# Performance work log

Hardware: AMD Instinct MI355X
Metric: run time of the kernel (lower is better)

## Reference

```python
import jax, jax.numpy as jnp
import numpy as np

N = 50000   # nodes
E = 800000  # edges (avg_degree 16)
C = 64      # channels
R = 8       # radial basis
H = 64      # radial MLP hidden
S = 10      # species
AVG_NUM_NEIGHBORS = 16.0


def setup_inputs() -> dict:
    key = jax.random.key(0)
    ks = jax.random.split(key, 16)
    node_feats0 = jax.random.normal(ks[0], (N, C), jnp.float32)
    node_feats1 = jax.random.normal(ks[1], (N, C, 3), jnp.float32)
    species = jax.random.randint(ks[2], (N,), 0, S)
    node_attrs = jax.nn.one_hot(species, S, dtype=jnp.float32)
    edge_index = jax.random.randint(ks[3], (2, E), 0, N)
    edge_feats = jax.random.normal(ks[4], (E, R), jnp.float32)
    vec = jax.random.normal(ks[5], (E, 3), jnp.float32)
    edge_attrs1 = vec / (jnp.linalg.norm(vec, axis=-1, keepdims=True) + 1e-9)
    cutoff = jax.random.uniform(ks[6], (E, 1), jnp.float32)
    Wup0 = jax.random.normal(ks[7], (C, C), jnp.float32) * (C ** -0.5)
    Wup1 = jax.random.normal(ks[8], (C, C), jnp.float32) * (C ** -0.5)
    W1 = jax.random.normal(ks[9], (R, H), jnp.float32) * (R ** -0.5)
    W2 = jax.random.normal(ks[10], (H, 4 * C), jnp.float32) * (H ** -0.5)
    Wsc0 = jax.random.normal(ks[11], (S, C, C), jnp.float32) * (C ** -0.5)
    Wsc1 = jax.random.normal(ks[12], (S, C, C), jnp.float32) * (C ** -0.5)
    Q0 = jnp.eye(1, dtype=jnp.float32)   # ICTD(0,0) projector
    Q1 = jnp.eye(3, dtype=jnp.float32)   # ICTD(1,1) projector
    return dict(node_feats0=node_feats0, node_feats1=node_feats1,
                node_attrs=node_attrs, edge_feats=edge_feats,
                edge_attrs1=edge_attrs1, cutoff=cutoff,
                Wup0=Wup0, Wup1=Wup1, W1=W1, W2=W2,
                Wsc0=Wsc0, Wsc1=Wsc1, Q0=Q0, Q1=Q1,
                edge_index=edge_index)


def reference(node_feats0, node_feats1, node_attrs, edge_feats, edge_attrs1,
              cutoff, Wup0, Wup1, W1, W2, Wsc0, Wsc1, Q0, Q1, edge_index):
    n = node_feats0.shape[0]
    src, dst = edge_index[0], edge_index[1]
    # linear_up (SelfInteraction): per-degree channel mixing
    h0 = node_feats0 @ Wup0                                   # [N,C]
    h1 = jnp.einsum('nci,co->noi', node_feats1, Wup1)         # [N,C,3]
    # radial MLP -> per-path per-channel edge weights
    w = jax.nn.silu(edge_feats @ W1) @ W2                     # [E,4C]
    w00, w11, w01, w10 = jnp.split(w, 4, axis=-1)             # each [E,C]
    # gather sender features per edge
    h0e = h0[src]                                             # [E,C]
    h1e = h1[src]                                             # [E,C,3]
    sh1 = edge_attrs1                                         # [E,3]
    # equivariant tensor-product paths, cutoff-modulated (Contraction)
    m0 = (w00 * h0e + w11 * jnp.einsum('eci,ei->ec', h1e, sh1)) * cutoff
    m1 = (w01[:, :, None] * h0e[:, :, None] * sh1[:, None, :]
          + w10[:, :, None] * h1e) * cutoff[:, :, None]       # [E,C,3]
    # scatter to receiver nodes + fixed normalizer
    T0 = jax.ops.segment_sum(m0, dst, num_segments=n) / AVG_NUM_NEIGHBORS
    T1 = jax.ops.segment_sum(m1, dst, num_segments=n) / AVG_NUM_NEIGHBORS
    # ICTD decomposition projection: T.reshape(B,C,-1) @ Q
    mi0 = (T0[:, :, None] @ Q0)[:, :, 0]                      # [N,C]
    mi1 = T1 @ Q1                                             # [N,C,3]
    # residual via ElementLinear (per-species channel mixing)
    res0 = jnp.einsum('ns,sco,nc->no', node_attrs, Wsc0, mi0)
    res1 = jnp.einsum('ns,sco,nci->noi', node_attrs, Wsc1, mi1)
    return jnp.concatenate(
        [mi0, mi1.reshape(n, 3 * C), res0, res1.reshape(n, 3 * C)], axis=-1)
```

## Files before the change

kernel.cpp:

```cpp
#include <hip/hip_runtime.h>
#include <math.h>


#define NB 16
#define TE 32

__device__ __forceinline__ float silu(float x) {
    return x / (1.0f + __expf(-x));
}

__global__ __launch_bounds__(256) void up_kernel(
    const float* __restrict__ nf0, const float* __restrict__ nf1,
    const float* __restrict__ Wup0, const float* __restrict__ Wup1,
    float* __restrict__ out, int Nn) {
    __shared__ float sW0[4096];
    __shared__ float sW1u[4096];
    __shared__ float s0[4 * 64];
    __shared__ float s1[4 * 192];
    int t = threadIdx.x;
    for (int i = t; i < 4096; i += 256) { sW0[i] = Wup0[i]; sW1u[i] = Wup1[i]; }
    int n0 = blockIdx.x * 4;
    {
        int n = n0 + (t >> 6);
        s0[t] = (n < Nn) ? nf0[(size_t)n * 64 + (t & 63)] : 0.f;
    }
    for (int i = t; i < 768; i += 256) {
        int n = n0 + i / 192;
        s1[i] = (n < Nn) ? nf1[(size_t)n * 192 + (i % 192)] : 0.f;
    }
    __syncthreads();
    int w = t >> 6, o = t & 63;
    int n = n0 + w;
    if (n >= Nn) return;
    float a0 = 0.f, ax = 0.f, ay = 0.f, az = 0.f;
#pragma unroll 8
    for (int c = 0; c < 64; c++) {
        float w0 = sW0[c * 64 + o];
        float w1 = sW1u[c * 64 + o];
        float f0 = s0[w * 64 + c];
        a0 += f0 * w0;
        ax += s1[w * 192 + c * 3 + 0] * w1;
        ay += s1[w * 192 + c * 3 + 1] * w1;
        az += s1[w * 192 + c * 3 + 2] * w1;
    }
    float* row = out + (size_t)n * 512;
    row[256 + o] = a0;
    row[320 + o * 3 + 0] = ax;
    row[320 + o * 3 + 1] = ay;
    row[320 + o * 3 + 2] = az;
}

__global__ __launch_bounds__(256) void hist_kernel(
    const int* __restrict__ ei, int* __restrict__ cnt, int E) {
    int e = blockIdx.x * 256 + threadIdx.x;
    if (e < E) atomicAdd(&cnt[ei[(size_t)E + e]], 1);
}

__global__ __launch_bounds__(1024) void scan_kernel(
    int* __restrict__ cnt, int* __restrict__ cur, int Nn, int E) {
    __shared__ int wsum[16];
    __shared__ int carry_s;
    int t = threadIdx.x;
    int lane = t & 63, wid = t >> 6;
    if (t == 0) carry_s = 0;
    __syncthreads();
    int nchunk = (Nn + 1023) >> 10;
    for (int ch = 0; ch < nchunk; ch++) {
        int i = (ch << 10) + t;
        int v = (i < Nn) ? cnt[i] : 0;
        int s = v;
#pragma unroll
        for (int d = 1; d < 64; d <<= 1) {
            int u = __shfl_up(s, d);
            if (lane >= d) s += u;
        }
        if (lane == 63) wsum[wid] = s;
        __syncthreads();
        int carry = carry_s;
        if (wid == 0) {
            int x = (lane < 16) ? wsum[lane] : 0;
#pragma unroll
            for (int d = 1; d < 16; d <<= 1) {
                int u = __shfl_up(x, d);
                if (lane >= d) x += u;
            }
            if (lane < 16) wsum[lane] = x;
        }
        __syncthreads();
        int woff = wid ? wsum[wid - 1] : 0;
        int excl = carry + woff + (s - v);
        if (i < Nn) { cnt[i] = excl; cur[i] = excl; }
        __syncthreads();
        if (t == 1023) carry_s = carry + wsum[15];
        __syncthreads();
    }
    if (t == 0) cnt[Nn] = E;
}

__global__ __launch_bounds__(256) void fill_kernel(
    const int* __restrict__ ei, int* __restrict__ cur, int* __restrict__ csr, int E) {
    int e = blockIdx.x * 256 + threadIdx.x;
    if (e < E) {
        int pos = atomicAdd(&cur[ei[(size_t)E + e]], 1);
        csr[pos] = e;
    }
}

#define FMA4(A, S, B) { (A).x += (S)*(B).x; (A).y += (S)*(B).y; (A).z += (S)*(B).z; (A).w += (S)*(B).w; }

__global__ __launch_bounds__(256, 1) void gather_kernel(
    const float* __restrict__ edge_feats, const float* __restrict__ edge_attrs1,
    const float* __restrict__ cutoff, const int* __restrict__ ei,
    const int* __restrict__ offs, const int* __restrict__ csr,
    const float* __restrict__ W1g, const float* __restrict__ W2g,
    float* __restrict__ out, int Nn, int E) {
    __shared__ __align__(16) float sW1[512];
    __shared__ __align__(16) float sW2[64 * 256];
    __shared__ __align__(16) float h_t[TE * 68];
    __shared__ __align__(16) float h0_t[TE * 68];
    __shared__ __align__(16) float h1_t[TE * 196];
    __shared__ __align__(16) float w_t[TE * 260];
    __shared__ __align__(16) float accs[NB * 256];
    __shared__ __align__(16) float4 meta4[TE];
    __shared__ int dstl[TE];
    int t = threadIdx.x;

    for (int i = t; i < 512; i += 256) sW1[i] = W1g[i];
    {
        float4* d4 = reinterpret_cast<float4*>(sW2);
        const float4* s4 = reinterpret_cast<const float4*>(W2g);
        for (int i = t; i < 4096; i += 256) d4[i] = s4[i];
    }
    for (int i = t; i < NB * 256; i += 256) accs[i] = 0.f;
    int n0 = blockIdx.x * NB;
    int nend = n0 + NB; if (nend > Nn) nend = Nn;
    int pbeg = offs[n0];
    int pend = offs[nend];
    __syncthreads();

    int e0 = t >> 3, q = t & 7;
    int g = t >> 5, cs = t & 31;
    int wv = t >> 6, c = t & 63;
    int off2 = (wv == 0) ? c : (64 + c * 3 + (wv - 1));

    const float4* h4  = reinterpret_cast<const float4*>(h_t);
    const float4* w24 = reinterpret_cast<const float4*>(sW2);
    float4* wt4 = reinterpret_cast<float4*>(w_t);

    float racc = 0.f;
    int prev = -1;

    for (int tb = pbeg; tb < pend; tb += TE) {
        int n_t = pend - tb; if (n_t > TE) n_t = TE;

        if (e0 < n_t) {
            int eg = csr[tb + e0];
            int src = ei[eg];
            if (q == 0) {
                dstl[e0] = ei[(size_t)E + eg] - n0;
                meta4[e0] = make_float4(edge_attrs1[(size_t)eg * 3 + 0],
                                        edge_attrs1[(size_t)eg * 3 + 1],
                                        edge_attrs1[(size_t)eg * 3 + 2],
                                        cutoff[eg]);
            }
            const float4* h0g = reinterpret_cast<const float4*>(out + (size_t)src * 512 + 256);
            const float4* h1g = reinterpret_cast<const float4*>(out + (size_t)src * 512 + 320);
            float4 ga = h0g[2 * q], gb = h0g[2 * q + 1];
            *reinterpret_cast<float4*>(&h0_t[e0 * 68 + q * 8]) = ga;
            *reinterpret_cast<float4*>(&h0_t[e0 * 68 + q * 8 + 4]) = gb;
#pragma unroll
            for (int k = 0; k < 6; k++) {
                float4 v = h1g[6 * q + k];
                *reinterpret_cast<float4*>(&h1_t[e0 * 196 + q * 24 + k * 4]) = v;
            }
            const float4* efp = reinterpret_cast<const float4*>(edge_feats + (size_t)eg * 8);
            float4 efa = efp[0], efb = efp[1];
            float hv0 = 0.f, hv1 = 0.f, hv2 = 0.f, hv3 = 0.f;
            float hv4 = 0.f, hv5 = 0.f, hv6 = 0.f, hv7 = 0.f;
            float4 wva, wvb;
#define H8(EFR, RR) \
            wva = *reinterpret_cast<const float4*>(&sW1[(RR) * 64 + q * 8]); \
            wvb = *reinterpret_cast<const float4*>(&sW1[(RR) * 64 + q * 8 + 4]); \
            hv0 += (EFR) * wva.x; hv1 += (EFR) * wva.y; hv2 += (EFR) * wva.z; hv3 += (EFR) * wva.w; \
            hv4 += (EFR) * wvb.x; hv5 += (EFR) * wvb.y; hv6 += (EFR) * wvb.z; hv7 += (EFR) * wvb.w;
            H8(efa.x, 0) H8(efa.y, 1) H8(efa.z, 2) H8(efa.w, 3)
            H8(efb.x, 4) H8(efb.y, 5) H8(efb.z, 6) H8(efb.w, 7)
#undef H8
            float4 o1 = make_float4(silu(hv0), silu(hv1), silu(hv2), silu(hv3));
            float4 o2 = make_float4(silu(hv4), silu(hv5), silu(hv6), silu(hv7));
            *reinterpret_cast<float4*>(&h_t[e0 * 68 + q * 8]) = o1;
            *reinterpret_cast<float4*>(&h_t[e0 * 68 + q * 8 + 4]) = o2;
        }
        __syncthreads();

        {
            float4 accA0 = {0,0,0,0}, accA1 = {0,0,0,0}, accA2 = {0,0,0,0}, accA3 = {0,0,0,0};
            float4 accB0 = {0,0,0,0}, accB1 = {0,0,0,0}, accB2 = {0,0,0,0}, accB3 = {0,0,0,0};
            int eb = g * 4;
#pragma unroll 4
            for (int lq = 0; lq < 16; lq++) {
                float4 ha0 = h4[(eb + 0) * 17 + lq];
                float4 ha1 = h4[(eb + 1) * 17 + lq];
                float4 ha2 = h4[(eb + 2) * 17 + lq];
                float4 ha3 = h4[(eb + 3) * 17 + lq];
#define S1LI(LI, CMP) { \
                float4 wA = w24[(lq * 4 + LI) * 64 + cs]; \
                float4 wB = w24[(lq * 4 + LI) * 64 + 32 + cs]; \
                FMA4(accA0, ha0.CMP, wA) FMA4(accB0, ha0.CMP, wB) \
                FMA4(accA1, ha1.CMP, wA) FMA4(accB1, ha1.CMP, wB) \
                FMA4(accA2, ha2.CMP, wA) FMA4(accB2, ha2.CMP, wB) \
                FMA4(accA3, ha3.CMP, wA) FMA4(accB3, ha3.CMP, wB) }
                S1LI(0, x) S1LI(1, y) S1LI(2, z) S1LI(3, w)
#undef S1LI
            }
            wt4[(eb + 0) * 65 + cs] = accA0; wt4[(eb + 0) * 65 + 32 + cs] = accB0;
            wt4[(eb + 1) * 65 + cs] = accA1; wt4[(eb + 1) * 65 + 32 + cs] = accB1;
            wt4[(eb + 2) * 65 + cs] = accA2; wt4[(eb + 2) * 65 + 32 + cs] = accB2;
            wt4[(eb + 3) * 65 + cs] = accA3; wt4[(eb + 3) * 65 + 32 + cs] = accB3;
        }
        __syncthreads();

        for (int e = 0; e < n_t; e++) {
            int d = dstl[e];
            float4 m = meta4[e];
            if (d != prev) {
                if (prev >= 0) atomicAdd(&accs[prev * 256 + off2], racc);
                racc = 0.f;
                prev = d;
            }
            float h0e = h0_t[e * 68 + c];
            if (wv == 0) {
                float w00 = w_t[e * 260 + c];
                float w11 = w_t[e * 260 + 64 + c];
                float x1 = h1_t[e * 196 + c * 3 + 0];
                float y1 = h1_t[e * 196 + c * 3 + 1];
                float z1 = h1_t[e * 196 + c * 3 + 2];
                float dd = x1 * m.x + y1 * m.y + z1 * m.z;
                racc += (w00 * h0e + w11 * dd) * m.w;
            } else {
                int i = wv - 1;
                float w01 = w_t[e * 260 + 128 + c];
                float w10 = w_t[e * 260 + 192 + c];
                float h1i = h1_t[e * 196 + c * 3 + i];
                float shi = (wv == 1) ? m.x : ((wv == 2) ? m.y : m.z);
                racc += (w01 * h0e * shi + w10 * h1i) * m.w;
            }
        }
        __syncthreads();
    }
    if (prev >= 0) atomicAdd(&accs[prev * 256 + off2], racc);
    __syncthreads();

    for (int i = t; i < NB * 256; i += 256) {
        int ln = i >> 8, idx = i & 255;
        if (n0 + ln < Nn) out[(size_t)(n0 + ln) * 512 + idx] = accs[i];
    }
}

__global__ __launch_bounds__(256, 2) void edge_kernel(
    const float* __restrict__ edge_feats, const float* __restrict__ edge_attrs1,
    const float* __restrict__ cutoff, const int* __restrict__ edge_index,
    const float* __restrict__ W1g, const float* __restrict__ W2g,
    float* __restrict__ out, int E) {
    __shared__ __align__(16) float sW1[8 * 64];
    __shared__ __align__(16) float sW2[64 * 256];
    int t = threadIdx.x;
    sW1[t] = W1g[t];
    sW1[t + 256] = W1g[t + 256];
    for (int i = t; i < 16384; i += 256) sW2[i] = W2g[i];
    __syncthreads();

    int e = blockIdx.x * 256 + t;
    if (e >= E) return;

    float ef[8];
    {
        const float4* p = reinterpret_cast<const float4*>(edge_feats + (size_t)e * 8);
        float4 a = p[0], b = p[1];
        ef[0] = a.x; ef[1] = a.y; ef[2] = a.z; ef[3] = a.w;
        ef[4] = b.x; ef[5] = b.y; ef[6] = b.z; ef[7] = b.w;
    }
    float h[64];
#pragma unroll
    for (int hg = 0; hg < 16; hg++) {
        float ax = 0.f, ay = 0.f, az = 0.f, aw = 0.f;
#pragma unroll
        for (int rr = 0; rr < 8; rr++) {
            const float4 wv = *reinterpret_cast<const float4*>(&sW1[rr * 64 + hg * 4]);
            ax += ef[rr] * wv.x; ay += ef[rr] * wv.y;
            az += ef[rr] * wv.z; aw += ef[rr] * wv.w;
        }
        h[hg * 4 + 0] = silu(ax);
        h[hg * 4 + 1] = silu(ay);
        h[hg * 4 + 2] = silu(az);
        h[hg * 4 + 3] = silu(aw);
    }

    int src = edge_index[e];
    int dst = edge_index[(size_t)E + e];
    float cut = cutoff[e];
    float sh0 = edge_attrs1[(size_t)e * 3 + 0];
    float sh1v = edge_attrs1[(size_t)e * 3 + 1];
    float sh2 = edge_attrs1[(size_t)e * 3 + 2];
    const float* h0r = out + (size_t)src * 512 + 256;
    const float* h1r = out + (size_t)src * 512 + 320;
    float* outr = out + (size_t)dst * 512;
    const float4* w2v = reinterpret_cast<const float4*>(sW2);

#pragma unroll 1
    for (int cg = 0; cg < 16; cg++) {
        float a00[4] = {0.f, 0.f, 0.f, 0.f};
        float a11[4] = {0.f, 0.f, 0.f, 0.f};
        float a01[4] = {0.f, 0.f, 0.f, 0.f};
        float a10[4] = {0.f, 0.f, 0.f, 0.f};
#pragma unroll
        for (int l = 0; l < 64; l++) {
            float hl = h[l];
            float4 w00v = w2v[l * 64 + cg];
            float4 w11v = w2v[l * 64 + 16 + cg];
            float4 w01v = w2v[l * 64 + 32 + cg];
            float4 w10v = w2v[l * 64 + 48 + cg];
            a00[0] += hl * w00v.x; a00[1] += hl * w00v.y; a00[2] += hl * w00v.z; a00[3] += hl * w00v.w;
            a11[0] += hl * w11v.x; a11[1] += hl * w11v.y; a11[2] += hl * w11v.z; a11[3] += hl * w11v.w;
            a01[0] += hl * w01v.x; a01[1] += hl * w01v.y; a01[2] += hl * w01v.z; a01[3] += hl * w01v.w;
            a10[0] += hl * w10v.x; a10[1] += hl * w10v.y; a10[2] += hl * w10v.z; a10[3] += hl * w10v.w;
        }
        int c0 = cg * 4;
        float4 h0v = *reinterpret_cast<const float4*>(h0r + c0);
        float4 q0 = *reinterpret_cast<const float4*>(h1r + c0 * 3);
        float4 q1 = *reinterpret_cast<const float4*>(h1r + c0 * 3 + 4);
        float4 q2 = *reinterpret_cast<const float4*>(h1r + c0 * 3 + 8);
        float h0a[4] = {h0v.x, h0v.y, h0v.z, h0v.w};
        float h1a[12] = {q0.x, q0.y, q0.z, q0.w, q1.x, q1.y, q1.z, q1.w,
                         q2.x, q2.y, q2.z, q2.w};
#pragma unroll
        for (int k = 0; k < 4; k++) {
            int c = c0 + k;
            float he0 = h0a[k];
            float e0 = h1a[k * 3 + 0], e1 = h1a[k * 3 + 1], e2 = h1a[k * 3 + 2];
            float d = e0 * sh0 + e1 * sh1v + e2 * sh2;
            float m0 = (a00[k] * he0 + a11[k] * d) * cut;
            atomicAdd(outr + c, m0);
            float wa = a01[k] * he0 * cut;
            float wb = a10[k] * cut;
            atomicAdd(outr + 64 + c * 3 + 0, wa * sh0 + wb * e0);
            atomicAdd(outr + 64 + c * 3 + 1, wa * sh1v + wb * e1);
            atomicAdd(outr + 64 + c * 3 + 2, wa * sh2 + wb * e2);
        }
    }
}

__global__ __launch_bounds__(256) void finalize_kernel(
    const float* __restrict__ node_attrs, const float* __restrict__ Wsc0,
    const float* __restrict__ Wsc1, const float* __restrict__ Q0,
    const float* __restrict__ Q1, float* __restrict__ out, int Nn) {
    __shared__ float smi0[4][64];
    __shared__ float smi1[4][192];
    int t = threadIdx.x;
    int w = t >> 6, o = t & 63;
    int n = blockIdx.x * 4 + w;
    const float inv = 1.0f / 16.0f;
    float q00 = Q0[0];
    float Q[9];
#pragma unroll
    for (int i = 0; i < 9; i++) Q[i] = Q1[i];
    if (n < Nn) {
        float* row = out + (size_t)n * 512;
        float t0 = row[o];
        float ta = row[64 + o * 3 + 0];
        float tb = row[64 + o * 3 + 1];
        float tc = row[64 + o * 3 + 2];
        float mi0 = t0 * inv * q00;
        float m0i = inv * (ta * Q[0] + tb * Q[3] + tc * Q[6]);
        float m1i = inv * (ta * Q[1] + tb * Q[4] + tc * Q[7]);
        float m2i = inv * (ta * Q[2] + tb * Q[5] + tc * Q[8]);
        row[o] = mi0;
        row[64 + o * 3 + 0] = m0i;
        row[64 + o * 3 + 1] = m1i;
        row[64 + o * 3 + 2] = m2i;
        smi0[w][o] = mi0;
        smi1[w][o * 3 + 0] = m0i;
        smi1[w][o * 3 + 1] = m1i;
        smi1[w][o * 3 + 2] = m2i;
    }
    __syncthreads();
    if (n >= Nn) return;
    float acc0 = 0.f, acc1x = 0.f, acc1y = 0.f, acc1z = 0.f;
    for (int s = 0; s < 10; s++) {
        float a = node_attrs[(size_t)n * 10 + s];
        if (a != 0.f) {
            const float* w0 = Wsc0 + s * 4096;
            const float* w1 = Wsc1 + s * 4096;
            float p0 = 0.f, px = 0.f, py = 0.f, pz = 0.f;
#pragma unroll 8
            for (int c = 0; c < 64; c++) {
                float v0 = w0[c * 64 + o];
                float v1 = w1[c * 64 + o];
                p0 += smi0[w][c] * v0;
                px += smi1[w][c * 3 + 0] * v1;
                py += smi1[w][c * 3 + 1] * v1;
                pz += smi1[w][c * 3 + 2] * v1;
            }
            acc0 += a * p0; acc1x += a * px; acc1y += a * py; acc1z += a * pz;
        }
    }
    float* row = out + (size_t)n * 512;
    row[256 + o] = acc0;
    row[320 + o * 3 + 0] = acc1x;
    row[320 + o * 3 + 1] = acc1y;
    row[320 + o * 3 + 2] = acc1z;
}

extern "C" void kernel_launch(void* const* d_in, const int* in_sizes, int n_in,
                              void* d_out, int out_size, void* d_ws, size_t ws_size,
                              hipStream_t stream) {
    const float* nf0   = (const float*)d_in[0];
    const float* nf1   = (const float*)d_in[1];
    const float* attrs = (const float*)d_in[2];
    const float* ef    = (const float*)d_in[3];
    const float* ea1   = (const float*)d_in[4];
    const float* cut   = (const float*)d_in[5];
    const float* Wup0  = (const float*)d_in[6];
    const float* Wup1  = (const float*)d_in[7];
    const float* W1    = (const float*)d_in[8];
    const float* W2    = (const float*)d_in[9];
    const float* Wsc0  = (const float*)d_in[10];
    const float* Wsc1  = (const float*)d_in[11];
    const float* Q0    = (const float*)d_in[12];
    const float* Q1    = (const float*)d_in[13];
    const int*   ei    = (const int*)d_in[14];
    int Nn = in_sizes[0] / 64;
    int E  = in_sizes[14] / 2;
    float* out = (float*)d_out;

    size_t need_bytes = ((size_t)(2 * Nn + 1) + (size_t)E) * sizeof(int);
    int ebl = (E + 255) / 256;

    if (d_ws != nullptr && ws_size >= need_bytes) {
        int* cnt = (int*)d_ws;
        int* cur = cnt + (Nn + 1);
        int* csr = cur + Nn;
        hipMemsetAsync(cnt, 0, (size_t)(Nn + 1) * sizeof(int), stream);
        hist_kernel<<<ebl, 256, 0, stream>>>(ei, cnt, E);
        scan_kernel<<<1, 1024, 0, stream>>>(cnt, cur, Nn, E);
        fill_kernel<<<ebl, 256, 0, stream>>>(ei, cur, csr, E);
        up_kernel<<<(Nn + 3) / 4, 256, 0, stream>>>(nf0, nf1, Wup0, Wup1, out, Nn);
        gather_kernel<<<(Nn + NB - 1) / NB, 256, 0, stream>>>(
            ef, ea1, cut, ei, cnt, csr, W1, W2, out, Nn, E);
        finalize_kernel<<<(Nn + 3) / 4, 256, 0, stream>>>(attrs, Wsc0, Wsc1, Q0, Q1, out, Nn);
    } else {
        hipMemsetAsync(out, 0, (size_t)out_size * sizeof(float), stream);
        up_kernel<<<(Nn + 3) / 4, 256, 0, stream>>>(nf0, nf1, Wup0, Wup1, out, Nn);
        edge_kernel<<<ebl, 256, 0, stream>>>(ef, ea1, cut, ei, W1, W2, out, E);
        finalize_kernel<<<(Nn + 3) / 4, 256, 0, stream>>>(attrs, Wsc0, Wsc1, Q0, Q1, out, Nn);
    }
}
```

Baseline: 1.825 ms.

## Prefetch next edge tile into registers and split scatter loop across waves by edge

Gathers for the next edge tile (source node features, edge features, attrs, cutoff, destination) are issued into registers right after the first barrier, so their global latency overlaps the W2 matmul stage of the current tile. The scatter-accumulate loop changes from each wave owning one output component over all edges to each wave taking every fourth edge and computing all four outputs. This removes redundant shared-memory reads and loop iterations per wave, but gives more flush points, issuing four shared atomics per destination change instead of one. The prefetch also raises register pressure under the 256-thread launch bound.

Result: faster. 1.605 ms (-12.1%).

```diff
diff --git a/kernel.cpp b/kernel.cpp
--- a/kernel.cpp
+++ b/kernel.cpp
@@ -141,40 +141,58 @@
     int e0 = t >> 3, q = t & 7;
     int g = t >> 5, cs = t & 31;
     int wv = t >> 6, c = t & 63;
-    int off2 = (wv == 0) ? c : (64 + c * 3 + (wv - 1));
 
     const float4* h4  = reinterpret_cast<const float4*>(h_t);
     const float4* w24 = reinterpret_cast<const float4*>(sW2);
     float4* wt4 = reinterpret_cast<float4*>(w_t);
 
-    float racc = 0.f;
+    float r0 = 0.f, rx = 0.f, ry = 0.f, rz = 0.f;
     int prev = -1;
 
-    for (int tb = pbeg; tb < pend; tb += TE) {
-        int n_t = pend - tb; if (n_t > TE) n_t = TE;
-
-        if (e0 < n_t) {
-            int eg = csr[tb + e0];
+    float4 pf_h0a, pf_h0b, pf_ef0, pf_ef1;
+    float4 pf_h10, pf_h11, pf_h12, pf_h13, pf_h14, pf_h15;
+    float4 pf_meta;
+    int pf_dst = 0;
+    bool pf_valid = false;
+
+    auto prefetch = [&](int tbn) {
+        int nt2 = pend - tbn; if (nt2 > TE) nt2 = TE;
+        pf_valid = (e0 < nt2);
+        if (pf_valid) {
+            int eg = csr[tbn + e0];
             int src = ei[eg];
             if (q == 0) {
-                dstl[e0] = ei[(size_t)E + eg] - n0;
-                meta4[e0] = make_float4(edge_attrs1[(size_t)eg * 3 + 0],
-                                        edge_attrs1[(size_t)eg * 3 + 1],
-                                        edge_attrs1[(size_t)eg * 3 + 2],
-                                        cutoff[eg]);
+                pf_dst = ei[(size_t)E + eg] - n0;
+                pf_meta = make_float4(edge_attrs1[(size_t)eg * 3 + 0],
+                                      edge_attrs1[(size_t)eg * 3 + 1],
+                                      edge_attrs1[(size_t)eg * 3 + 2],
+                                      cutoff[eg]);
             }
             const float4* h0g = reinterpret_cast<const float4*>(out + (size_t)src * 512 + 256);
             const float4* h1g = reinterpret_cast<const float4*>(out + (size_t)src * 512 + 320);
-            float4 ga = h0g[2 * q], gb = h0g[2 * q + 1];
-            *reinterpret_cast<float4*>(&h0_t[e0 * 68 + q * 8]) = ga;
-            *reinterpret_cast<float4*>(&h0_t[e0 * 68 + q * 8 + 4]) = gb;
-#pragma unroll
-            for (int k = 0; k < 6; k++) {
-                float4 v = h1g[6 * q + k];
-                *reinterpret_cast<float4*>(&h1_t[e0 * 196 + q * 24 + k * 4]) = v;
-            }
+            pf_h0a = h0g[2 * q]; pf_h0b = h0g[2 * q + 1];
+            pf_h10 = h1g[6 * q + 0]; pf_h11 = h1g[6 * q + 1]; pf_h12 = h1g[6 * q + 2];
+            pf_h13 = h1g[6 * q + 3]; pf_h14 = h1g[6 * q + 4]; pf_h15 = h1g[6 * q + 5];
             const float4* efp = reinterpret_cast<const float4*>(edge_feats + (size_t)eg * 8);
-            float4 efa = efp[0], efb = efp[1];
+            pf_ef0 = efp[0]; pf_ef1 = efp[1];
+        }
+    };
+
+    prefetch(pbeg);
+
+    for (int tb = pbeg; tb < pend; tb += TE) {
+        int n_t = pend - tb; if (n_t > TE) n_t = TE;
+
+        if (pf_valid) {
+            if (q == 0) { dstl[e0] = pf_dst; meta4[e0] = pf_meta; }
+            *reinterpret_cast<float4*>(&h0_t[e0 * 68 + q * 8]) = pf_h0a;
+            *reinterpret_cast<float4*>(&h0_t[e0 * 68 + q * 8 + 4]) = pf_h0b;
+            *reinterpret_cast<float4*>(&h1_t[e0 * 196 + q * 24 + 0])  = pf_h10;
+            *reinterpret_cast<float4*>(&h1_t[e0 * 196 + q * 24 + 4])  = pf_h11;
+            *reinterpret_cast<float4*>(&h1_t[e0 * 196 + q * 24 + 8])  = pf_h12;
+            *reinterpret_cast<float4*>(&h1_t[e0 * 196 + q * 24 + 12]) = pf_h13;
+            *reinterpret_cast<float4*>(&h1_t[e0 * 196 + q * 24 + 16]) = pf_h14;
+            *reinterpret_cast<float4*>(&h1_t[e0 * 196 + q * 24 + 20]) = pf_h15;
             float hv0 = 0.f, hv1 = 0.f, hv2 = 0.f, hv3 = 0.f;
             float hv4 = 0.f, hv5 = 0.f, hv6 = 0.f, hv7 = 0.f;
             float4 wva, wvb;
@@ -183,8 +201,8 @@
             wvb = *reinterpret_cast<const float4*>(&sW1[(RR) * 64 + q * 8 + 4]); \
             hv0 += (EFR) * wva.x; hv1 += (EFR) * wva.y; hv2 += (EFR) * wva.z; hv3 += (EFR) * wva.w; \
             hv4 += (EFR) * wvb.x; hv5 += (EFR) * wvb.y; hv6 += (EFR) * wvb.z; hv7 += (EFR) * wvb.w;
-            H8(efa.x, 0) H8(efa.y, 1) H8(efa.z, 2) H8(efa.w, 3)
-            H8(efb.x, 4) H8(efb.y, 5) H8(efb.z, 6) H8(efb.w, 7)
+            H8(pf_ef0.x, 0) H8(pf_ef0.y, 1) H8(pf_ef0.z, 2) H8(pf_ef0.w, 3)
+            H8(pf_ef1.x, 4) H8(pf_ef1.y, 5) H8(pf_ef1.z, 6) H8(pf_ef1.w, 7)
 #undef H8
             float4 o1 = make_float4(silu(hv0), silu(hv1), silu(hv2), silu(hv3));
             float4 o2 = make_float4(silu(hv4), silu(hv5), silu(hv6), silu(hv7));
@@ -192,6 +210,8 @@
             *reinterpret_cast<float4*>(&h_t[e0 * 68 + q * 8 + 4]) = o2;
         }
         __syncthreads();
+
+        if (tb + TE < pend) prefetch(tb + TE); else pf_valid = false;
 
         {
             float4 accA0 = {0,0,0,0}, accA1 = {0,0,0,0}, accA2 = {0,0,0,0}, accA3 = {0,0,0,0};
@@ -220,35 +240,43 @@
         }
         __syncthreads();
 
-        for (int e = 0; e < n_t; e++) {
+        for (int e = wv; e < n_t; e += 4) {
             int d = dstl[e];
             float4 m = meta4[e];
             if (d != prev) {
-                if (prev >= 0) atomicAdd(&accs[prev * 256 + off2], racc);
-                racc = 0.f;
+                if (prev >= 0) {
+                    atomicAdd(&accs[prev * 256 + c], r0);
+                    atomicAdd(&accs[prev * 256 + 64 + c * 3 + 0], rx);
+                    atomicAdd(&accs[prev * 256 + 64 + c * 3 + 1], ry);
+                    atomicAdd(&accs[prev * 256 + 64 + c * 3 + 2], rz);
+                }
+                r0 = rx = ry = rz = 0.f;
                 prev = d;
             }
             float h0e = h0_t[e * 68 + c];
-            if (wv == 0) {
-                float w00 = w_t[e * 260 + c];
-                float w11 = w_t[e * 260 + 64 + c];
-                float x1 = h1_t[e * 196 + c * 3 + 0];
-                float y1 = h1_t[e * 196 + c * 3 + 1];
-                float z1 = h1_t[e * 196 + c * 3 + 2];
-                float dd = x1 * m.x + y1 * m.y + z1 * m.z;
-                racc += (w00 * h0e + w11 * dd) * m.w;
-            } else {
-                int i = wv - 1;
-                float w01 = w_t[e * 260 + 128 + c];
-                float w10 = w_t[e * 260 + 192 + c];
-                float h1i = h1_t[e * 196 + c * 3 + i];
-                float shi = (wv == 1) ? m.x : ((wv == 2) ? m.y : m.z);
-                racc += (w01 * h0e * shi + w10 * h1i) * m.w;
-            }
-        }
-        __syncthreads();
-    }
-    if (prev >= 0) atomicAdd(&accs[prev * 256 + off2], racc);
+            float w00 = w_t[e * 260 + c];
+            float w11 = w_t[e * 260 + 64 + c];
+            float w01 = w_t[e * 260 + 128 + c];
+            float w10 = w_t[e * 260 + 192 + c];
+            float x1 = h1_t[e * 196 + c * 3 + 0];
+            float y1 = h1_t[e * 196 + c * 3 + 1];
+            float z1 = h1_t[e * 196 + c * 3 + 2];
+            float dd = x1 * m.x + y1 * m.y + z1 * m.z;
+            r0 += (w00 * h0e + w11 * dd) * m.w;
+            float wa = w01 * h0e * m.w;
+            float wb = w10 * m.w;
+            rx += wa * m.x + wb * x1;
+            ry += wa * m.y + wb * y1;
+            rz += wa * m.z + wb * z1;
+        }
+        __syncthreads();
+    }
+    if (prev >= 0) {
+        atomicAdd(&accs[prev * 256 + c], r0);
+        atomicAdd(&accs[prev * 256 + 64 + c * 3 + 0], rx);
+        atomicAdd(&accs[prev * 256 + 64 + c * 3 + 1], ry);
+        atomicAdd(&accs[prev * 256 + 64 + c * 3 + 2], rz);
+    }
     __syncthreads();
 
     for (int i = t; i < NB * 256; i += 256) {
```
